# Kernel optimization log

Hardware: AMD Instinct MI355X
Metric: run time of the kernel (lower is better)

Reference implementation:

```python
import jax, jax.numpy as jnp
import numpy as np

E = 8            # num_experts
PS = 8           # patch size (fixed across layers since ps-2 < 8)
F = 6            # fourier frequencies
CC = 4 + 8 * F   # coord feature channels = 52
RH = 16          # router hidden channels (embed_dim)
TEMP = 1.0
THRESH = 0.05
LAYERS = [(3, 8), (8, 16), (16, 16), (16, 32)]  # (C_in, C_out) per layer
NUM_CLASSES = 100


def coord_features(H, W, ps, nf):
    # [4+8F, H, W]: global (x,y) + patch-local (x,y) + sin/cos fourier bands
    gy = (jnp.arange(H, dtype=jnp.float32) + 0.5) / H
    gx = (jnp.arange(W, dtype=jnp.float32) + 0.5) / W
    ly = ((jnp.arange(H) % ps).astype(jnp.float32) + 0.5) / ps
    lx = ((jnp.arange(W) % ps).astype(jnp.float32) + 0.5) / ps
    Gy = jnp.broadcast_to(gy[:, None], (H, W))
    Gx = jnp.broadcast_to(gx[None, :], (H, W))
    Ly = jnp.broadcast_to(ly[:, None], (H, W))
    Lx = jnp.broadcast_to(lx[None, :], (H, W))
    base = jnp.stack([Gx, Gy, Lx, Ly], 0)  # [4,H,W]
    bands = [base]
    for f in range(nf):
        w = (2.0 ** f) * jnp.pi
        bands.append(jnp.sin(w * base))
        bands.append(jnp.cos(w * base))
    return jnp.concatenate(bands, 0)


def patchify(x, ps):
    B, C, H, W = x.shape
    h, w = H // ps, W // ps
    x = x.reshape(B, C, h, ps, w, ps).transpose(0, 2, 4, 1, 3, 5)
    return x.reshape(B, h * w, C, ps, ps), h, w


def unpatchify(x, h, w):
    # 'b (h w) c ph pw -> b c (h ph) (w pw)'
    B, P, C, ph, pw = x.shape
    return x.reshape(B, h, w, C, ph, pw).transpose(0, 3, 1, 4, 2, 5).reshape(B, C, h * ph, w * pw)


def pce_layer(X, ew, eb, rw, rb, rlw, rlb):
    B, C, H, W = X.shape
    Xp, h, w = patchify(X, PS)             # [B,P,C,ps,ps]
    P = h * w
    Xf = Xp.reshape(B * P, C, PS, PS)
    coords = coord_features(H, W, PS, F)   # [CC,H,W] (same for every image)
    Cp, _, _ = patchify(coords[None], PS)
    Cp = Cp[0]                             # [P,CC,ps,ps]
    # Router: 1x1 conv proj -> ReLU -> global avg pool -> linear -> softmax/temp -> threshold + renorm
    z = jax.nn.relu(jnp.einsum('rc,pcij->prij', rw, Cp) + rb[None, :, None, None])
    z = z.mean((2, 3))                     # [P,RH]
    logits = z @ rlw.T + rlb               # [P,E]
    probs = jax.nn.softmax(logits / TEMP, axis=-1)
    keep = (probs >= THRESH).astype(probs.dtype)
    probs = probs * keep
    probs = probs / (probs.sum(-1, keepdims=True) + 1e-9)
    scores = jnp.broadcast_to(probs[None], (B, P, E))  # [B,P,E]
    # Dense all-experts conv: stack experts along output channels of one conv
    y = jax.lax.conv_general_dilated(Xf, ew, (1, 1), 'SAME',
                                     dimension_numbers=('NCHW', 'OIHW', 'NCHW'))
    y = jax.nn.relu(y + eb[None, :, None, None])       # [B*P, E*Cout, ps, ps]
    Cout = ew.shape[0] // E
    y = y.reshape(B, P, E, Cout, PS, PS)
    out = jnp.einsum('bpecij,bpe->bpcij', y, scores)   # weighted combine over experts
    return unpatchify(out, h, w)


def setup_inputs() -> dict:
    key = jax.random.key(0)
    ks = jax.random.split(key, 32)
    d = {'X': jax.random.normal(ks[0], (16, 3, 128, 128), dtype=jnp.float32)}
    ki = 1
    for li, (cin, cout) in enumerate(LAYERS):
        d[f'ew{li}'] = jax.random.normal(ks[ki], (E * cout, cin, 3, 3), dtype=jnp.float32) * (1.0 / np.sqrt(cin * 9)); ki += 1
        d[f'eb{li}'] = jax.random.normal(ks[ki], (E * cout,), dtype=jnp.float32) * 0.01; ki += 1
        d[f'rw{li}'] = jax.random.normal(ks[ki], (RH, CC), dtype=jnp.float32) * (1.0 / np.sqrt(CC)); ki += 1
        d[f'rb{li}'] = jax.random.normal(ks[ki], (RH,), dtype=jnp.float32) * 0.01; ki += 1
        d[f'rlw{li}'] = jax.random.normal(ks[ki], (E, RH), dtype=jnp.float32) * (1.0 / np.sqrt(RH)); ki += 1
        d[f'rlb{li}'] = jax.random.normal(ks[ki], (E,), dtype=jnp.float32) * 0.01; ki += 1
    d['fcw'] = jax.random.normal(ks[ki], (NUM_CLASSES, LAYERS[-1][1] * 8 * 8), dtype=jnp.float32) * 0.02; ki += 1
    d['fcb'] = jnp.zeros((NUM_CLASSES,), dtype=jnp.float32)
    return d


def reference(X, ew0, eb0, rw0, rb0, rlw0, rlb0,
              ew1, eb1, rw1, rb1, rlw1, rlb1,
              ew2, eb2, rw2, rb2, rlw2, rlb2,
              ew3, eb3, rw3, rb3, rlw3, rlb3,
              fcw, fcb):
    layer_params = [(ew0, eb0, rw0, rb0, rlw0, rlb0),
                    (ew1, eb1, rw1, rb1, rlw1, rlb1),
                    (ew2, eb2, rw2, rb2, rlw2, rlb2),
                    (ew3, eb3, rw3, rb3, rlw3, rlb3)]
    for p in layer_params:
        X = pce_layer(X, *p)
    B, C, H, W = X.shape
    # AdaptiveAvgPool2d(8): exact 16x16 mean pooling for 128x128
    pooled = X.reshape(B, C, 8, H // 8, 8, W // 8).mean((3, 5))
    flat = pooled.reshape(B, -1)
    return flat @ fcw.T + fcb
```

## Files before the change

kernel.cpp:

```cpp
#include <hip/hip_runtime.h>
#include <math.h>

#define NE 8
#define PI_F 3.14159265358979323846f

typedef _Float16 half8 __attribute__((ext_vector_type(8)));
typedef float f32x4 __attribute__((ext_vector_type(4)));
typedef float f32x16 __attribute__((ext_vector_type(16)));
typedef unsigned int uint2v __attribute__((ext_vector_type(2)));
typedef unsigned int u32x4 __attribute__((ext_vector_type(4)));
typedef unsigned short u16x4 __attribute__((ext_vector_type(4)));

#define CP 24
#define ROWS 240
#define NELEM 2400

__device__ __forceinline__ unsigned short f2h_bits(float v) {
    union { _Float16 h; unsigned short u; } cv;
    cv.h = (_Float16)v;
    return cv.u;
}

struct SetupArgs {
    const float* rw[4]; const float* rb[4]; const float* rlw[4]; const float* rlb[4];
    const float* ew[4];
    float* probs;
    unsigned short* w0; unsigned short* w1; unsigned short* w2; unsigned short* w3;
};

template<int CIN, int CSTR, int KSL>
__device__ __forceinline__ void prep_one32(
    const float* __restrict__ ew, unsigned short* __restrict__ wA, int idx)
{
    int j    = idx & 7;
    int lane = (idx >> 3) & 63;
    int t2   = idx >> 9;
    int ks   = t2 % KSL;
    int mt   = t2 / KSL;
    int m    = mt * 32 + (lane & 31);
    int k    = ks * 16 + (lane >> 5) * 8 + j;
    int cin  = k % CSTR, r = k / CSTR;
    float val = 0.0f;
    if (cin < CIN && r < 9)
        val = ew[((size_t)m * CIN + cin) * 9 + r];
    wA[idx] = f2h_bits(val);
}

__global__ __launch_bounds__(256) void setup_all(SetupArgs sa)
{
    int bx = blockIdx.x, tid = threadIdx.x;
    if (bx < 256) {
        int layer = tid >> 6, lane = tid & 63;
        const float* rw  = sa.rw[layer];  const float* rb  = sa.rb[layer];
        const float* rlw = sa.rlw[layer]; const float* rlb = sa.rlb[layer];
        int p = bx, py = p >> 4, px = p & 15;
        int i = lane >> 3, j = lane & 7;
        int y = py * 8 + i, x = px * 8 + j;

        float base0 = (x + 0.5f) / 128.0f;
        float base1 = (y + 0.5f) / 128.0f;
        float base2 = (j + 0.5f) / 8.0f;
        float base3 = (i + 0.5f) / 8.0f;

        float coord[52];
        coord[0] = base0; coord[1] = base1; coord[2] = base2; coord[3] = base3;
        int c = 4;
        #pragma unroll
        for (int f = 0; f < 6; ++f) {
            float w = PI_F * (float)(1 << f);
            coord[c+0] = sinf(w * base0); coord[c+1] = sinf(w * base1);
            coord[c+2] = sinf(w * base2); coord[c+3] = sinf(w * base3);
            coord[c+4] = cosf(w * base0); coord[c+5] = cosf(w * base1);
            coord[c+6] = cosf(w * base2); coord[c+7] = cosf(w * base3);
            c += 8;
        }
        float z[16];
        #pragma unroll
        for (int r = 0; r < 16; ++r) {
            float a = rb[r];
            #pragma unroll
            for (int cc = 0; cc < 52; ++cc) a += rw[r*52 + cc] * coord[cc];
            z[r] = fmaxf(a, 0.0f);
        }
        #pragma unroll
        for (int r = 0; r < 16; ++r) {
            float v = z[r];
            #pragma unroll
            for (int off = 32; off > 0; off >>= 1) v += __shfl_xor(v, off);
            z[r] = v * (1.0f / 64.0f);
        }
        int e = lane & 7;
        float logit = rlb[e];
        #pragma unroll
        for (int r = 0; r < 16; ++r) logit += rlw[e*16 + r] * z[r];
        float m = logit;
        #pragma unroll
        for (int off = 4; off > 0; off >>= 1) m = fmaxf(m, __shfl_xor(m, off));
        float ex = expf(logit - m);
        float s = ex;
        #pragma unroll
        for (int off = 4; off > 0; off >>= 1) s += __shfl_xor(s, off);
        float pr = ex / s;
        pr = (pr >= 0.05f) ? pr : 0.0f;
        float s2 = pr;
        #pragma unroll
        for (int off = 4; off > 0; off >>= 1) s2 += __shfl_xor(s2, off);
        pr = pr / (s2 + 1e-9f);
        if (lane < 8) sa.probs[layer * 2048 + p * 8 + lane] = pr;
    } else {
        int idx = (bx - 256) * 256 + tid;
        if (idx < 3072)       prep_one32<3, 4, 3>(sa.ew[0], sa.w0, idx);
        else if (idx < 13312) prep_one32<8, 8, 5>(sa.ew[1], sa.w1, idx - 3072);
        else if (idx < 31744) prep_one32<16, 16, 9>(sa.ew[2], sa.w2, idx - 13312);
        else if (idx < 68608) prep_one32<16, 16, 9>(sa.ew[3], sa.w3, idx - 31744);
    }
}

template<int KSL, int CSTR>
__device__ __forceinline__ void build_B32(
    half8* B, const unsigned short* ain, int n, int hi)
{
    int pr = n >> 3, pc = n & 7;
    int rbase = pr * ROWS + pc * CP;
    if (CSTR == 16) {
        #pragma unroll
        for (int ks = 0; ks < KSL; ++ks) {
            int off = ((ks / 3) * 10 + (ks % 3)) * CP + hi * 8;
            B[ks] = *(const half8*)(ain + rbase + off);
        }
    } else if (CSTR == 8) {
        #pragma unroll
        for (int ks = 0; ks < KSL; ++ks) {
            int r0 = 2 * ks, r1 = 2 * ks + 1;
            int o0 = ((r0 / 3) * 10 + (r0 % 3)) * CP;
            int o1 = (r1 < 9) ? ((r1 / 3) * 10 + (r1 % 3)) * CP : 0;
            int off = hi ? o1 : o0;
            half8 v{};
            if (2 * ks + hi < 9) v = *(const half8*)(ain + rbase + off);
            B[ks] = v;
        }
    } else {
        #pragma unroll
        for (int ks = 0; ks < KSL; ++ks) {
            union { half8 v; uint2v u2[2]; } bb;
            #pragma unroll
            for (int h = 0; h < 2; ++h) {
                int ra = 4 * ks + h;
                int rb_ = 4 * ks + 2 + h;
                int oa = (ra < 9) ? ((ra / 3) * 10 + (ra % 3)) * CP : 0;
                int ob = (rb_ < 9) ? ((rb_ / 3) * 10 + (rb_ % 3)) * CP : 0;
                int r = 4 * ks + 2 * hi + h;
                int off = hi ? ob : oa;
                uint2v u{};
                if (r < 9) u = *(const uint2v*)(ain + rbase + off);
                bb.u2[h] = u;
            }
            B[ks] = bb.v;
        }
    }
}

template<int KSL, int CSTR, int MT, int CPE, bool LAST>
__device__ __forceinline__ void layer32(
    unsigned short* Aw,
    const unsigned short* __restrict__ wA,
    const float* sbR_L, const float* se_L,
    int l, int hi, int l31, float* pout)
{
    int n0 = l31, n1 = 32 + l31;
    half8 B0[KSL], B1[KSL];
    build_B32<KSL, CSTR>(B0, Aw, n0, hi);
    build_B32<KSL, CSTR>(B1, Aw, n1, hi);

    constexpr int KH0 = (KSL + 1) / 2;
    constexpr int KH1 = KSL - KH0;

    f32x16 accL = {0.f};
    f32x4 acc0a = {0,0,0,0}, acc0b = {0,0,0,0};
    f32x4 acc1a = {0,0,0,0}, acc1b = {0,0,0,0};
    f32x4 acc0s = {0,0,0,0}, acc1s = {0,0,0,0};

    const unsigned short* apl = wA + l * 8;
    half8 A0[KH0], A1[KH1 > 0 ? KH1 : 1];
    #pragma unroll
    for (int q = 0; q < KH0; ++q)
        A0[q] = *(const half8*)(apl + q * 512);

    #pragma unroll 1
    for (int mt = 0; mt < MT; ++mt) {
        const unsigned short* base = apl + mt * (KSL * 512);
        #pragma unroll
        for (int q = 0; q < KH1; ++q)
            A1[q] = *(const half8*)(base + (KH0 + q) * 512);

        const float* bp = sbR_L + mt * 32 + hi * 16;
        f32x4 b0 = *(const f32x4*)(bp);
        f32x4 b1 = *(const f32x4*)(bp + 4);
        f32x4 b2 = *(const f32x4*)(bp + 8);
        f32x4 b3 = *(const f32x4*)(bp + 12);
        f32x16 ct0;
        #pragma unroll
        for (int i = 0; i < 4; ++i) {
            ct0[i] = b0[i]; ct0[4+i] = b1[i]; ct0[8+i] = b2[i]; ct0[12+i] = b3[i];
        }
        f32x16 ct1 = ct0;

        #pragma unroll
        for (int q = 0; q < KH0; ++q) {
            ct0 = __builtin_amdgcn_mfma_f32_32x32x16_f16(A0[q], B0[q], ct0, 0, 0, 0);
            ct1 = __builtin_amdgcn_mfma_f32_32x32x16_f16(A0[q], B1[q], ct1, 0, 0, 0);
        }

        const unsigned short* nbase = apl + ((mt + 1 < MT) ? (mt + 1) : 0) * (KSL * 512);
        #pragma unroll
        for (int q = 0; q < KH0; ++q)
            A0[q] = *(const half8*)(nbase + q * 512);

        #pragma unroll
        for (int q = 0; q < KH1; ++q) {
            ct0 = __builtin_amdgcn_mfma_f32_32x32x16_f16(A1[q], B0[KH0 + q], ct0, 0, 0, 0);
            ct1 = __builtin_amdgcn_mfma_f32_32x32x16_f16(A1[q], B1[KH0 + q], ct1, 0, 0, 0);
        }

        if (CPE == 32) {
            float pe = se_L[mt];
            #pragma unroll
            for (int g = 0; g < 16; ++g)
                accL[g] = fmaf(fmaxf(ct0[g], 0.f) + fmaxf(ct1[g], 0.f), pe, accL[g]);
        } else if (CPE == 16) {
            float pe0 = se_L[2 * mt], pe1 = se_L[2 * mt + 1];
            #pragma unroll
            for (int g = 0; g < 4; ++g) {
                acc0a[g] = fmaf(fmaxf(ct0[g],      0.f), pe0, acc0a[g]);
                acc0a[g] = fmaf(fmaxf(ct0[8 + g],  0.f), pe1, acc0a[g]);
                acc0b[g] = fmaf(fmaxf(ct0[4 + g],  0.f), pe0, acc0b[g]);
                acc0b[g] = fmaf(fmaxf(ct0[12 + g], 0.f), pe1, acc0b[g]);
                acc1a[g] = fmaf(fmaxf(ct1[g],      0.f), pe0, acc1a[g]);
                acc1a[g] = fmaf(fmaxf(ct1[8 + g],  0.f), pe1, acc1a[g]);
                acc1b[g] = fmaf(fmaxf(ct1[4 + g],  0.f), pe0, acc1b[g]);
                acc1b[g] = fmaf(fmaxf(ct1[12 + g], 0.f), pe1, acc1b[g]);
            }
        } else {
            #pragma unroll
            for (int q = 0; q < 4; ++q) {
                float pe = se_L[4 * mt + q];
                #pragma unroll
                for (int g = 0; g < 4; ++g) {
                    acc0s[g] = fmaf(fmaxf(ct0[4 * q + g], 0.f), pe, acc0s[g]);
                    acc1s[g] = fmaf(fmaxf(ct1[4 * q + g], 0.f), pe, acc1s[g]);
                }
            }
        }
    }

    if (!LAST) {
        int wb0 = (1 + (n0 >> 3)) * ROWS + (1 + (n0 & 7)) * CP;
        int wb1 = (1 + (n1 >> 3)) * ROWS + (1 + (n1 & 7)) * CP;
        union { _Float16 h[4]; u16x4 u; } o;
        if (CPE == 8) {
            #pragma unroll
            for (int g = 0; g < 4; ++g) o.h[g] = (_Float16)acc0s[g];
            *(u16x4*)(Aw + wb0 + 4 * hi) = o.u;
            #pragma unroll
            for (int g = 0; g < 4; ++g) o.h[g] = (_Float16)acc1s[g];
            *(u16x4*)(Aw + wb1 + 4 * hi) = o.u;
        } else {
            #pragma unroll
            for (int g = 0; g < 4; ++g) o.h[g] = (_Float16)acc0a[g];
            *(u16x4*)(Aw + wb0 + 4 * hi) = o.u;
            #pragma unroll
            for (int g = 0; g < 4; ++g) o.h[g] = (_Float16)acc0b[g];
            *(u16x4*)(Aw + wb0 + 8 + 4 * hi) = o.u;
            #pragma unroll
            for (int g = 0; g < 4; ++g) o.h[g] = (_Float16)acc1a[g];
            *(u16x4*)(Aw + wb1 + 4 * hi) = o.u;
            #pragma unroll
            for (int g = 0; g < 4; ++g) o.h[g] = (_Float16)acc1b[g];
            *(u16x4*)(Aw + wb1 + 8 + 4 * hi) = o.u;
        }
    } else {
        #pragma unroll
        for (int g = 0; g < 16; ++g) {
            float s = accL[g];
            s += __shfl_xor(s, 1);  s += __shfl_xor(s, 2);
            s += __shfl_xor(s, 4);  s += __shfl_xor(s, 8);
            s += __shfl_xor(s, 16);
            accL[g] = s;
        }
        if (l31 == 0) {
            #pragma unroll
            for (int qd = 0; qd < 4; ++qd) {
                f32x4 v = { accL[4*qd], accL[4*qd+1], accL[4*qd+2], accL[4*qd+3] };
                *(f32x4*)(pout + qd * 8 + 4 * hi) = v;
            }
        }
    }
}

__global__ __launch_bounds__(128, 2) void pce_fused(
    const float* __restrict__ X,
    const unsigned short* __restrict__ wA0, const unsigned short* __restrict__ wA1,
    const unsigned short* __restrict__ wA2, const unsigned short* __restrict__ wA3,
    const float* __restrict__ eb0, const float* __restrict__ eb1,
    const float* __restrict__ eb2, const float* __restrict__ eb3,
    const float* __restrict__ probs,
    float* __restrict__ psums)
{
    int bx = blockIdx.x;
    int b = bx >> 7;
    int pbase = (bx & 127) << 1;
    int tid = threadIdx.x;
    int w = tid >> 6, l = tid & 63;
    int p = pbase + w;
    int py = p >> 4, px = p & 15;

    __shared__ alignas(16) unsigned short A[2][NELEM];
    __shared__ alignas(16) float sbR[576];
    __shared__ alignas(16) float se[4][2][8];

    if (tid < 64) {
        int layer = tid >> 4, q = (tid >> 3) & 1, e = tid & 7;
        se[layer][q][e] = probs[layer * 2048 + (pbase + q) * 8 + e];
    }
    for (int t = tid; t < 576; t += 128) {
        const float* ebp; int off;
        if (t < 64)       { ebp = eb0; off = 0; }
        else if (t < 192) { ebp = eb1; off = 64; }
        else if (t < 320) { ebp = eb2; off = 192; }
        else              { ebp = eb3; off = 320; }
        int local = t - off;
        int mt = local >> 5, q = local & 31;
        int hi2 = q >> 4, reg = q & 15;
        int row = (reg & 3) + 8 * (reg >> 2) + 4 * hi2;
        sbR[t] = ebp[mt * 32 + row];
    }

    unsigned short* Aw = A[w];
    {
        u32x4 z = {0u, 0u, 0u, 0u};
        for (int t = l; t < 300; t += 64) ((u32x4*)Aw)[t] = z;
        for (int t = l; t < 192; t += 64) {
            int cin = t >> 6, pix = t & 63, i = pix >> 3, j = pix & 7;
            float v = X[((size_t)(b * 3 + cin) * 128 + (py * 8 + i)) * 128 + (px * 8 + j)];
            Aw[(1 + i) * ROWS + (1 + j) * CP + cin] = f2h_bits(v);
        }
    }
    __syncthreads();

    int l31 = l & 31, hi = l >> 5;
    float* pout = psums + (size_t)(b * 256 + p) * 32;

    layer32<3, 4, 2, 8, false>(Aw, wA0, sbR,       se[0][w], l, hi, l31, nullptr);
    layer32<5, 8, 4, 16, false>(Aw, wA1, sbR + 64,  se[1][w], l, hi, l31, nullptr);
    layer32<9, 16, 4, 16, false>(Aw, wA2, sbR + 192, se[2][w], l, hi, l31, nullptr);
    layer32<9, 16, 8, 32, true>(Aw, wA3, sbR + 320, se[3][w], l, hi, l31, pout);
}

__global__ __launch_bounds__(256) void fc_kernel(
    const float* __restrict__ psums, const float* __restrict__ fcw,
    const float* __restrict__ fcb, float* __restrict__ out)
{
    int b = blockIdx.x >> 3, chunk = blockIdx.x & 7;
    __shared__ float pooled[2048];
    for (int t = threadIdx.x; t < 2048; t += 256) {
        int c = t >> 6, cell = t & 63, oy = cell >> 3, ox = cell & 7;
        float s = 0.0f;
        #pragma unroll
        for (int dy = 0; dy < 2; ++dy)
            #pragma unroll
            for (int dx = 0; dx < 2; ++dx) {
                int pp = (2 * oy + dy) * 16 + (2 * ox + dx);
                s += psums[(size_t)(b * 256 + pp) * 32 + c];
            }
        pooled[t] = s * (1.0f / 256.0f);
    }
    __syncthreads();

    int wave = threadIdx.x >> 6, lane = threadIdx.x & 63;
    for (int ci = wave; ci < 13; ci += 4) {
        int cls = chunk * 13 + ci;
        if (cls < 100) {
            float a = 0.0f;
            #pragma unroll
            for (int r = 0; r < 32; ++r)
                a += pooled[r * 64 + lane] * fcw[(size_t)cls * 2048 + r * 64 + lane];
            #pragma unroll
            for (int off = 32; off > 0; off >>= 1) a += __shfl_down(a, off);
            if (lane == 0) out[b * 100 + cls] = a + fcb[cls];
        }
    }
}

extern "C" void kernel_launch(void* const* d_in, const int* in_sizes, int n_in,
                              void* d_out, int out_size, void* d_ws, size_t ws_size,
                              hipStream_t stream) {
    const float* X = (const float*)d_in[0];
    const float* eb[4];
    SetupArgs sa;
    for (int l = 0; l < 4; ++l) {
        sa.ew[l]  = (const float*)d_in[1 + 6*l + 0];
        eb[l]     = (const float*)d_in[1 + 6*l + 1];
        sa.rw[l]  = (const float*)d_in[1 + 6*l + 2];
        sa.rb[l]  = (const float*)d_in[1 + 6*l + 3];
        sa.rlw[l] = (const float*)d_in[1 + 6*l + 4];
        sa.rlb[l] = (const float*)d_in[1 + 6*l + 5];
    }
    const float* fcw = (const float*)d_in[25];
    const float* fcb = (const float*)d_in[26];

    char* ws = (char*)d_ws;
    float* probs  = (float*)ws;
    float* psums  = (float*)(ws + 32768);
    unsigned short* wA0 = (unsigned short*)(ws + 32768 + 524288);
    unsigned short* wA1 = wA0 + 3072;
    unsigned short* wA2 = wA1 + 10240;
    unsigned short* wA3 = wA2 + 18432;

    sa.probs = probs; sa.w0 = wA0; sa.w1 = wA1; sa.w2 = wA2; sa.w3 = wA3;

    setup_all<<<524, 256, 0, stream>>>(sa);
    pce_fused<<<2048, 128, 0, stream>>>(X, wA0, wA1, wA2, wA3,
                                        eb[0], eb[1], eb[2], eb[3], probs, psums);
    fc_kernel<<<128, 256, 0, stream>>>(psums, fcw, fcb, (float*)d_out);
}
```

Baseline: 76.31 us.

## Split layer compute into per-N-tile passes with ping-pong LDS buffers

Each layer now processes its two 32-column output tiles in two sequential passes instead of holding both B fragments and accumulators at once, cutting live registers roughly in half. Because the in-place overwrite no longer works when tiles are processed separately, activations ping-pong between two LDS buffers per wave. Launch bounds move from 2 to 3 blocks per SIMD to take advantage of the lower register pressure. In exchange, LDS use doubles, A-weight loads from global/L2 are issued twice per layer, and MFMA chains are shorter with less interleaving between independent accumulators.

```diff
diff --git a/kernel.cpp b/kernel.cpp
--- a/kernel.cpp
+++ b/kernel.cpp
@@ -161,24 +161,21 @@
 }
 
 template<int KSL, int CSTR, int MT, int CPE, bool LAST>
-__device__ __forceinline__ void layer32(
-    unsigned short* Aw,
+__device__ __forceinline__ void layer_nt(
+    const unsigned short* Ain, unsigned short* Aout,
     const unsigned short* __restrict__ wA,
     const float* sbR_L, const float* se_L,
-    int l, int hi, int l31, float* pout)
-{
-    int n0 = l31, n1 = 32 + l31;
-    half8 B0[KSL], B1[KSL];
-    build_B32<KSL, CSTR>(B0, Aw, n0, hi);
-    build_B32<KSL, CSTR>(B1, Aw, n1, hi);
+    int l, int hi, int l31, int nt, f32x16& accL)
+{
+    int n = nt * 32 + l31;
+    half8 B[KSL];
+    build_B32<KSL, CSTR>(B, Ain, n, hi);
 
     constexpr int KH0 = (KSL + 1) / 2;
     constexpr int KH1 = KSL - KH0;
 
-    f32x16 accL = {0.f};
-    f32x4 acc0a = {0,0,0,0}, acc0b = {0,0,0,0};
-    f32x4 acc1a = {0,0,0,0}, acc1b = {0,0,0,0};
-    f32x4 acc0s = {0,0,0,0}, acc1s = {0,0,0,0};
+    f32x4 acc_a = {0,0,0,0}, acc_b = {0,0,0,0};
+    f32x4 acc_s = {0,0,0,0};
 
     const unsigned short* apl = wA + l * 8;
     half8 A0[KH0], A1[KH1 > 0 ? KH1 : 1];
@@ -198,18 +195,15 @@
         f32x4 b1 = *(const f32x4*)(bp + 4);
         f32x4 b2 = *(const f32x4*)(bp + 8);
         f32x4 b3 = *(const f32x4*)(bp + 12);
-        f32x16 ct0;
+        f32x16 ct;
         #pragma unroll
         for (int i = 0; i < 4; ++i) {
-            ct0[i] = b0[i]; ct0[4+i] = b1[i]; ct0[8+i] = b2[i]; ct0[12+i] = b3[i];
-        }
-        f32x16 ct1 = ct0;
-
-        #pragma unroll
-        for (int q = 0; q < KH0; ++q) {
-            ct0 = __builtin_amdgcn_mfma_f32_32x32x16_f16(A0[q], B0[q], ct0, 0, 0, 0);
-            ct1 = __builtin_amdgcn_mfma_f32_32x32x16_f16(A0[q], B1[q], ct1, 0, 0, 0);
-        }
+            ct[i] = b0[i]; ct[4+i] = b1[i]; ct[8+i] = b2[i]; ct[12+i] = b3[i];
+        }
+
+        #pragma unroll
+        for (int q = 0; q < KH0; ++q)
+            ct = __builtin_amdgcn_mfma_f32_32x32x16_f16(A0[q], B[q], ct, 0, 0, 0);
 
         const unsigned short* nbase = apl + ((mt + 1 < MT) ? (mt + 1) : 0) * (KSL * 512);
         #pragma unroll
@@ -217,87 +211,53 @@
             A0[q] = *(const half8*)(nbase + q * 512);
 
         #pragma unroll
-        for (int q = 0; q < KH1; ++q) {
-            ct0 = __builtin_amdgcn_mfma_f32_32x32x16_f16(A1[q], B0[KH0 + q], ct0, 0, 0, 0);
-            ct1 = __builtin_amdgcn_mfma_f32_32x32x16_f16(A1[q], B1[KH0 + q], ct1, 0, 0, 0);
-        }
+        for (int q = 0; q < KH1; ++q)
+            ct = __builtin_amdgcn_mfma_f32_32x32x16_f16(A1[q], B[KH0 + q], ct, 0, 0, 0);
 
         if (CPE == 32) {
             float pe = se_L[mt];
             #pragma unroll
             for (int g = 0; g < 16; ++g)
-                accL[g] = fmaf(fmaxf(ct0[g], 0.f) + fmaxf(ct1[g], 0.f), pe, accL[g]);
+                accL[g] = fmaf(fmaxf(ct[g], 0.f), pe, accL[g]);
         } else if (CPE == 16) {
             float pe0 = se_L[2 * mt], pe1 = se_L[2 * mt + 1];
             #pragma unroll
             for (int g = 0; g < 4; ++g) {
-                acc0a[g] = fmaf(fmaxf(ct0[g],      0.f), pe0, acc0a[g]);
-                acc0a[g] = fmaf(fmaxf(ct0[8 + g],  0.f), pe1, acc0a[g]);
-                acc0b[g] = fmaf(fmaxf(ct0[4 + g],  0.f), pe0, acc0b[g]);
-                acc0b[g] = fmaf(fmaxf(ct0[12 + g], 0.f), pe1, acc0b[g]);
-                acc1a[g] = fmaf(fmaxf(ct1[g],      0.f), pe0, acc1a[g]);
-                acc1a[g] = fmaf(fmaxf(ct1[8 + g],  0.f), pe1, acc1a[g]);
-                acc1b[g] = fmaf(fmaxf(ct1[4 + g],  0.f), pe0, acc1b[g]);
-                acc1b[g] = fmaf(fmaxf(ct1[12 + g], 0.f), pe1, acc1b[g]);
+                acc_a[g] = fmaf(fmaxf(ct[g],      0.f), pe0, acc_a[g]);
+                acc_a[g] = fmaf(fmaxf(ct[8 + g],  0.f), pe1, acc_a[g]);
+                acc_b[g] = fmaf(fmaxf(ct[4 + g],  0.f), pe0, acc_b[g]);
+                acc_b[g] = fmaf(fmaxf(ct[12 + g], 0.f), pe1, acc_b[g]);
             }
         } else {
             #pragma unroll
             for (int q = 0; q < 4; ++q) {
                 float pe = se_L[4 * mt + q];
                 #pragma unroll
-                for (int g = 0; g < 4; ++g) {
-                    acc0s[g] = fmaf(fmaxf(ct0[4 * q + g], 0.f), pe, acc0s[g]);
-                    acc1s[g] = fmaf(fmaxf(ct1[4 * q + g], 0.f), pe, acc1s[g]);
-                }
+                for (int g = 0; g < 4; ++g)
+                    acc_s[g] = fmaf(fmaxf(ct[4 * q + g], 0.f), pe, acc_s[g]);
             }
         }
     }
 
     if (!LAST) {
-        int wb0 = (1 + (n0 >> 3)) * ROWS + (1 + (n0 & 7)) * CP;
-        int wb1 = (1 + (n1 >> 3)) * ROWS + (1 + (n1 & 7)) * CP;
+        int wb = (1 + (n >> 3)) * ROWS + (1 + (n & 7)) * CP;
         union { _Float16 h[4]; u16x4 u; } o;
         if (CPE == 8) {
             #pragma unroll
-            for (int g = 0; g < 4; ++g) o.h[g] = (_Float16)acc0s[g];
-            *(u16x4*)(Aw + wb0 + 4 * hi) = o.u;
-            #pragma unroll
-            for (int g = 0; g < 4; ++g) o.h[g] = (_Float16)acc1s[g];
-            *(u16x4*)(Aw + wb1 + 4 * hi) = o.u;
+            for (int g = 0; g < 4; ++g) o.h[g] = (_Float16)acc_s[g];
+            *(u16x4*)(Aout + wb + 4 * hi) = o.u;
         } else {
             #pragma unroll
-            for (int g = 0; g < 4; ++g) o.h[g] = (_Float16)acc0a[g];
-            *(u16x4*)(Aw + wb0 + 4 * hi) = o.u;
-            #pragma unroll
-            for (int g = 0; g < 4; ++g) o.h[g] = (_Float16)acc0b[g];
-            *(u16x4*)(Aw + wb0 + 8 + 4 * hi) = o.u;
-            #pragma unroll
-            for (int g = 0; g < 4; ++g) o.h[g] = (_Float16)acc1a[g];
-            *(u16x4*)(Aw + wb1 + 4 * hi) = o.u;
-            #pragma unroll
-            for (int g = 0; g < 4; ++g) o.h[g] = (_Float16)acc1b[g];
-            *(u16x4*)(Aw + wb1 + 8 + 4 * hi) = o.u;
-        }
-    } else {
-        #pragma unroll
-        for (int g = 0; g < 16; ++g) {
-            float s = accL[g];
-            s += __shfl_xor(s, 1);  s += __shfl_xor(s, 2);
-            s += __shfl_xor(s, 4);  s += __shfl_xor(s, 8);
-            s += __shfl_xor(s, 16);
-            accL[g] = s;
-        }
-        if (l31 == 0) {
-            #pragma unroll
-            for (int qd = 0; qd < 4; ++qd) {
-                f32x4 v = { accL[4*qd], accL[4*qd+1], accL[4*qd+2], accL[4*qd+3] };
-                *(f32x4*)(pout + qd * 8 + 4 * hi) = v;
-            }
-        }
-    }
-}
-
-__global__ __launch_bounds__(128, 2) void pce_fused(
+            for (int g = 0; g < 4; ++g) o.h[g] = (_Float16)acc_a[g];
+            *(u16x4*)(Aout + wb + 4 * hi) = o.u;
+            #pragma unroll
+            for (int g = 0; g < 4; ++g) o.h[g] = (_Float16)acc_b[g];
+            *(u16x4*)(Aout + wb + 8 + 4 * hi) = o.u;
+        }
+    }
+}
+
+__global__ __launch_bounds__(128, 3) void pce_fused(
     const float* __restrict__ X,
     const unsigned short* __restrict__ wA0, const unsigned short* __restrict__ wA1,
     const unsigned short* __restrict__ wA2, const unsigned short* __restrict__ wA3,
@@ -314,7 +274,7 @@
     int p = pbase + w;
     int py = p >> 4, px = p & 15;
 
-    __shared__ alignas(16) unsigned short A[2][NELEM];
+    __shared__ alignas(16) unsigned short A[2][2][NELEM];
     __shared__ alignas(16) float sbR[576];
     __shared__ alignas(16) float se[4][2][8];
 
@@ -335,25 +295,50 @@
         sbR[t] = ebp[mt * 32 + row];
     }
 
-    unsigned short* Aw = A[w];
+    unsigned short* Aping = A[w][0];
+    unsigned short* Apong = A[w][1];
     {
         u32x4 z = {0u, 0u, 0u, 0u};
-        for (int t = l; t < 300; t += 64) ((u32x4*)Aw)[t] = z;
+        for (int t = l; t < 300; t += 64) {
+            ((u32x4*)Aping)[t] = z;
+            ((u32x4*)Apong)[t] = z;
+        }
         for (int t = l; t < 192; t += 64) {
             int cin = t >> 6, pix = t & 63, i = pix >> 3, j = pix & 7;
             float v = X[((size_t)(b * 3 + cin) * 128 + (py * 8 + i)) * 128 + (px * 8 + j)];
-            Aw[(1 + i) * ROWS + (1 + j) * CP + cin] = f2h_bits(v);
+            Aping[(1 + i) * ROWS + (1 + j) * CP + cin] = f2h_bits(v);
         }
     }
     __syncthreads();
 
     int l31 = l & 31, hi = l >> 5;
+    f32x16 accL = {0.f};
+
+    layer_nt<3, 4, 2, 8, false>(Aping, Apong, wA0, sbR,       se[0][w], l, hi, l31, 0, accL);
+    layer_nt<3, 4, 2, 8, false>(Aping, Apong, wA0, sbR,       se[0][w], l, hi, l31, 1, accL);
+    layer_nt<5, 8, 4, 16, false>(Apong, Aping, wA1, sbR + 64,  se[1][w], l, hi, l31, 0, accL);
+    layer_nt<5, 8, 4, 16, false>(Apong, Aping, wA1, sbR + 64,  se[1][w], l, hi, l31, 1, accL);
+    layer_nt<9, 16, 4, 16, false>(Aping, Apong, wA2, sbR + 192, se[2][w], l, hi, l31, 0, accL);
+    layer_nt<9, 16, 4, 16, false>(Aping, Apong, wA2, sbR + 192, se[2][w], l, hi, l31, 1, accL);
+    layer_nt<9, 16, 8, 32, true>(Apong, Aping, wA3, sbR + 320, se[3][w], l, hi, l31, 0, accL);
+    layer_nt<9, 16, 8, 32, true>(Apong, Aping, wA3, sbR + 320, se[3][w], l, hi, l31, 1, accL);
+
     float* pout = psums + (size_t)(b * 256 + p) * 32;
-
-    layer32<3, 4, 2, 8, false>(Aw, wA0, sbR,       se[0][w], l, hi, l31, nullptr);
-    layer32<5, 8, 4, 16, false>(Aw, wA1, sbR + 64,  se[1][w], l, hi, l31, nullptr);
-    layer32<9, 16, 4, 16, false>(Aw, wA2, sbR + 192, se[2][w], l, hi, l31, nullptr);
-    layer32<9, 16, 8, 32, true>(Aw, wA3, sbR + 320, se[3][w], l, hi, l31, pout);
+    #pragma unroll
+    for (int g = 0; g < 16; ++g) {
+        float s = accL[g];
+        s += __shfl_xor(s, 1);  s += __shfl_xor(s, 2);
+        s += __shfl_xor(s, 4);  s += __shfl_xor(s, 8);
+        s += __shfl_xor(s, 16);
+        accL[g] = s;
+    }
+    if (l31 == 0) {
+        #pragma unroll
+        for (int qd = 0; qd < 4; ++qd) {
+            f32x4 v = { accL[4*qd], accL[4*qd+1], accL[4*qd+2], accL[4*qd+3] };
+            *(f32x4*)(pout + qd * 8 + 4 * hi) = v;
+        }
+    }
 }
 
 __global__ __launch_bounds__(256) void fc_kernel(
```

Result: slower. 80.12 us (+5.0%).
